# Performance work log

Measured on AMD Instinct MI355X. Metric: run time of the kernel, lower is better.

## Reference

```python
import jax, jax.numpy as jnp
import numpy as np

EPS = 1e-12  # matches torch F.normalize eps
TEMPERATURE = 1.0
LAMBDA = 0.8


def _l2norm(x):
    n = jnp.sqrt(jnp.sum(x * x, axis=-1, keepdims=True))
    return x / jnp.maximum(n, EPS)


def setup_inputs() -> dict:
    key = jax.random.key(0)
    feats = jax.random.normal(key, (4, 4096, 512), dtype=jnp.float32)
    return {"feats": feats, "node": 8}


def reference(feats, node):
    f = _l2norm(feats)                                   # [B,N,D]
    scores = jnp.einsum('bnd,bmd->bnm', f, f) / TEMPERATURE  # [B,N,N]
    vals, idx = jax.lax.top_k(scores, node)              # [B,N,k]
    B, N, _ = scores.shape
    bi = jnp.arange(B)[:, None, None]
    ni = jnp.arange(N)[None, :, None]
    sparse = jnp.full_like(scores, -jnp.inf).at[bi, ni, idx].set(vals)
    w = jax.nn.softmax(sparse, axis=-1)                  # zeros outside top-k
    feats_att = jnp.einsum('bnm,bmd->bnd', w, f)
    feats_gam = f * LAMBDA + feats_att * (1.0 - LAMBDA)
    return _l2norm(feats_gam)
```

## Files before the change

kernel.cpp:

```cpp
#include <hip/hip_runtime.h>
#include <stdint.h>

#define NROWS 4096
#define NDIM  512
#define TOPT  8
#define NLIST 16
#define NCAND 128
#define NRESC 12
#define KSEL  8

typedef __attribute__((ext_vector_type(8))) short short8;
typedef __attribute__((ext_vector_type(4))) float f32x4;

__device__ __forceinline__ unsigned short f2bf(float x) {
  unsigned int u = __float_as_uint(x);
  return (unsigned short)((u + 0x7fffu + ((u >> 16) & 1u)) >> 16);
}

__device__ __forceinline__ void gl_lds16(const void* g, void* l) {
  void* gnc = (void*)g;
  __builtin_amdgcn_global_load_lds(
      (__attribute__((address_space(1))) void*)gnc,
      (__attribute__((address_space(3))) void*)l, 16, 0, 0);
}

__device__ __forceinline__ void ins8(unsigned int (&tv)[TOPT], unsigned int k) {
#pragma unroll
  for (int j = 0; j < TOPT; ++j) {
    const unsigned int nt = tv[j] > k ? tv[j] : k;
    k = tv[j] > k ? k : tv[j];
    tv[j] = nt;
  }
}

__global__ __launch_bounds__(256) void k_norm(const float* __restrict__ in,
                                              float* __restrict__ fout,
                                              unsigned short* __restrict__ fbf) {
  const int row = blockIdx.x * 4 + (threadIdx.x >> 6);
  const int l = threadIdx.x & 63;
  const float4* src = reinterpret_cast<const float4*>(in + (size_t)row * NDIM);
  float4 a = src[l * 2], b = src[l * 2 + 1];
  float ss = a.x * a.x + a.y * a.y + a.z * a.z + a.w * a.w +
             b.x * b.x + b.y * b.y + b.z * b.z + b.w * b.w;
#pragma unroll
  for (int off = 32; off; off >>= 1) ss += __shfl_xor(ss, off, 64);
  const float inv = 1.0f / fmaxf(sqrtf(ss), 1e-12f);
  a.x *= inv; a.y *= inv; a.z *= inv; a.w *= inv;
  b.x *= inv; b.y *= inv; b.z *= inv; b.w *= inv;
  float4* dst = reinterpret_cast<float4*>(fout + (size_t)row * NDIM);
  dst[l * 2] = a; dst[l * 2 + 1] = b;
  uint4 ub;
  ub.x = (unsigned)f2bf(a.x) | ((unsigned)f2bf(a.y) << 16);
  ub.y = (unsigned)f2bf(a.z) | ((unsigned)f2bf(a.w) << 16);
  ub.z = (unsigned)f2bf(b.x) | ((unsigned)f2bf(b.y) << 16);
  ub.w = (unsigned)f2bf(b.z) | ((unsigned)f2bf(b.w) << 16);
  reinterpret_cast<uint4*>(fbf + (size_t)row * NDIM)[l] = ub;
}

__global__ __launch_bounds__(512, 4) void k_coarse(const unsigned short* __restrict__ fbf,
                                                   unsigned int* __restrict__ keys) {
  __shared__ alignas(16) union {
    struct { unsigned short A[128 * 64]; unsigned short B[128 * 64]; } st;
    unsigned short S[128 * 128];
  } sh;

  const int tid = threadIdx.x;
  const int w = tid >> 6, l = tid & 63;

  const int lin = blockIdx.x;
  const int xcd = lin & 7;
  const int slot = lin >> 3;
  const int xq = xcd * 4 + (slot & 3);
  const int ym = (slot >> 2) & 7;
  const int zb = slot >> 5;

  const int q0 = xq * 128;
  const int m0 = ym * 512;
  const int bbase = zb * NROWS;

  const int qh = w >> 2, mq = w & 3;
  const int r = tid >> 2, sub = tid & 3;
  const int rx = r & 31;

  const int lrow = (l >> 3);
  const int lkg  = ((l & 7) ^ lrow) * 8;

  unsigned int tv[TOPT];
#pragma unroll
  for (int j = 0; j < TOPT; ++j) tv[j] = 0u;

  const f32x4 vzero = {0.f, 0.f, 0.f, 0.f};

  for (int mt = 0; mt < 4; ++mt) {
    const int mbase = m0 + mt * 128;
    f32x4 acc[4][2];
#pragma unroll
    for (int i = 0; i < 4; ++i)
#pragma unroll
      for (int j = 0; j < 2; ++j) acc[i][j] = vzero;

    for (int kt = 0; kt < 8; ++kt) {
      const int kk = kt * 64;
#pragma unroll
      for (int t = 0; t < 2; ++t) {
        const int sa = w * 2 + t;
        const int srow = sa * 8 + lrow;
        gl_lds16(fbf + ((size_t)(bbase + q0 + srow) << 9) + kk + lkg,
                 &sh.st.A[sa * 512]);
        gl_lds16(fbf + ((size_t)(bbase + mbase + srow) << 9) + kk + lkg,
                 &sh.st.B[sa * 512]);
      }
      __syncthreads();
#pragma unroll
      for (int ks = 0; ks < 2; ++ks) {
        short8 av[4], bv[2];
        const int kgrp = ks * 4 + (l >> 4);
#pragma unroll
        for (int i = 0; i < 4; ++i) {
          const int row = qh * 64 + i * 16 + (l & 15);
          av[i] = *(const short8*)&sh.st.A[row * 64 + (kgrp ^ (l & 7)) * 8];
        }
#pragma unroll
        for (int j = 0; j < 2; ++j) {
          const int row = mq * 32 + j * 16 + (l & 15);
          bv[j] = *(const short8*)&sh.st.B[row * 64 + (kgrp ^ (l & 7)) * 8];
        }
#pragma unroll
        for (int i = 0; i < 4; ++i)
#pragma unroll
          for (int j = 0; j < 2; ++j)
            acc[i][j] = __builtin_amdgcn_mfma_f32_16x16x32_bf16(av[i], bv[j], acc[i][j], 0, 0, 0);
      }
      __syncthreads();
    }

#pragma unroll
    for (int i = 0; i < 4; ++i) {
      const int qb_ = qh * 64 + i * 16 + (l >> 4) * 4;
#pragma unroll
      for (int j = 0; j < 2; ++j) {
        const int mc = mq * 32 + j * 16 + (l & 15);
#pragma unroll
        for (int rr = 0; rr < 4; ++rr) {
          const int q = qb_ + rr;
          unsigned int uu = __float_as_uint(acc[i][j][rr]);
          uu ^= (unsigned int)(((int)uu) >> 31) | 0x80000000u;
          const int pg = ((mc >> 2) ^ (q & 31));
          sh.S[q * 128 + pg * 4 + (mc & 3)] = (unsigned short)(uu >> 16);
        }
      }
    }
    __syncthreads();

    {
      const int invb0 = 4095 - (mbase + sub * 32);
#pragma unroll 4
      for (int cg = 0; cg < 8; ++cg) {
        const int pg = (sub * 8 + cg) ^ rx;
        const ushort4 s4 = *(const ushort4*)&sh.S[r * 128 + pg * 4];
        const unsigned int invb = (unsigned int)(invb0 - cg * 4);
        const unsigned int k0 = ((unsigned int)s4.x << 16) | invb;
        const unsigned int k1 = ((unsigned int)s4.y << 16) | (invb - 1);
        const unsigned int k2 = ((unsigned int)s4.z << 16) | (invb - 2);
        const unsigned int k3 = ((unsigned int)s4.w << 16) | (invb - 3);
        if (k0 > tv[TOPT - 1]) ins8(tv, k0);
        if (k1 > tv[TOPT - 1]) ins8(tv, k1);
        if (k2 > tv[TOPT - 1]) ins8(tv, k2);
        if (k3 > tv[TOPT - 1]) ins8(tv, k3);
      }
    }
    __syncthreads();
  }

  unsigned int ov[TOPT];
#pragma unroll
  for (int j = 0; j < TOPT; ++j) ov[j] = __shfl_xor(tv[j], 1, 64);
  unsigned int mg[TOPT];
#pragma unroll
  for (int j = 0; j < TOPT; ++j) {
    const unsigned int o = ov[TOPT - 1 - j];
    mg[j] = tv[j] > o ? tv[j] : o;
  }

  if ((sub & 1) == 0) {
    const int list = ym * 2 + (sub >> 1);
    unsigned int* dst = keys + (((size_t)(bbase + q0 + r)) * NLIST + list) * TOPT;
    reinterpret_cast<uint4*>(dst)[0] = make_uint4(mg[0], mg[1], mg[2], mg[3]);
    reinterpret_cast<uint4*>(dst)[1] = make_uint4(mg[4], mg[5], mg[6], mg[7]);
  }
}

__global__ __launch_bounds__(256) void k_final(const float* __restrict__ f,
                                               const unsigned int* __restrict__ keys,
                                               float* __restrict__ out) {
  __shared__ int sh_si[4][NRESC];

  const int lin = blockIdx.x;
  const int xcd = lin & 7;
  const int slot = lin >> 3;
  const int b = xcd >> 1;
  const int wv = threadIdx.x >> 6;
  const int n = ((xcd & 1) * 512 + slot) * 4 + wv;
  const int qg = b * NROWS + n;
  const int l = threadIdx.x & 63;

  const uint2 kk = reinterpret_cast<const uint2*>(keys + (size_t)qg * NCAND)[l];
  const unsigned int ka = kk.x, kb = kk.y;

  unsigned int T = 0u;
#pragma unroll
  for (int bit = 31; bit >= 0; --bit) {
    const unsigned int Tp = T | (1u << bit);
    const int cnt = (int)__popcll(__ballot(ka >= Tp)) +
                    (int)__popcll(__ballot(kb >= Tp));
    T = (cnt >= NRESC) ? Tp : T;
  }

  {
    const unsigned long long mA = __ballot(ka >= T);
    const unsigned long long mB = __ballot(kb >= T);
    const unsigned long long lt = (1ull << l) - 1ull;
    if (ka >= T) sh_si[wv][(int)__popcll(mA & lt)] = 4095 - (int)(ka & 4095u);
    if (kb >= T) sh_si[wv][(int)__popcll(mA) + (int)__popcll(mB & lt)] =
        4095 - (int)(kb & 4095u);
  }
  asm volatile("s_waitcnt lgkmcnt(0)" ::: "memory");
  __builtin_amdgcn_sched_barrier(0);

  int si[NRESC];
#pragma unroll
  for (int j = 0; j < NRESC; ++j)
    si[j] = __builtin_amdgcn_readfirstlane(sh_si[wv][j]);

  const float* __restrict__ fb = f + (size_t)b * NROWS * NDIM;
  const float* frow = fb + (size_t)n * NDIM;
  float selfv[8];
#pragma unroll
  for (int c = 0; c < 8; ++c) selfv[c] = frow[c * 64 + l];

  double ex[NRESC];
#pragma unroll
  for (int rr = 0; rr < NRESC; ++rr) {
    const float* g = fb + (size_t)si[rr] * NDIM;
    double s = 0.0;
#pragma unroll
    for (int c = 0; c < 8; ++c) s += (double)selfv[c] * (double)g[c * 64 + l];
    ex[rr] = s;
  }
#pragma unroll
  for (int off = 32; off; off >>= 1) {
#pragma unroll
    for (int rr = 0; rr < NRESC; ++rr) ex[rr] += __shfl_xor(ex[rr], off, 64);
  }

  int rank_[NRESC];
#pragma unroll
  for (int j = 0; j < NRESC; ++j) {
    int rk = 0;
#pragma unroll
    for (int a = 0; a < NRESC; ++a) {
      if (a != j) {
        const bool beats = (ex[a] > ex[j]) || (ex[a] == ex[j] && si[a] < si[j]);
        rk += beats ? 1 : 0;
      }
    }
    rank_[j] = rk;
  }
  double mxd = ex[0];
#pragma unroll
  for (int j = 1; j < NRESC; ++j) mxd = ex[j] > mxd ? ex[j] : mxd;

  const float mxf = (float)mxd;
  float wj[NRESC];
  float wsum = 0.f;
#pragma unroll
  for (int j = 0; j < NRESC; ++j) {
    const float e = expf((float)ex[j] - mxf);
    wj[j] = (rank_[j] < KSEL) ? e : 0.f;
    wsum += wj[j];
  }
  const float cs = 0.2f / wsum;

  float acc[8];
#pragma unroll
  for (int c = 0; c < 8; ++c) acc[c] = 0.8f * selfv[c];
#pragma unroll
  for (int rr = 0; rr < NRESC; ++rr) {
    if (rank_[rr] < KSEL) {
      const float* g = fb + (size_t)si[rr] * NDIM;
      const float wr = cs * wj[rr];
#pragma unroll
      for (int c = 0; c < 8; ++c) acc[c] = fmaf(wr, g[c * 64 + l], acc[c]);
    }
  }

  float ss = 0.f;
#pragma unroll
  for (int c = 0; c < 8; ++c) ss += acc[c] * acc[c];
#pragma unroll
  for (int off = 32; off; off >>= 1) ss += __shfl_xor(ss, off, 64);
  const float inv = 1.0f / fmaxf(sqrtf(ss), 1e-12f);
  float* orow = out + (size_t)qg * NDIM;
#pragma unroll
  for (int c = 0; c < 8; ++c) orow[c * 64 + l] = acc[c] * inv;
}

extern "C" void kernel_launch(void* const* d_in, const int* in_sizes, int n_in,
                              void* d_out, int out_size, void* d_ws, size_t ws_size,
                              hipStream_t stream) {
  (void)in_sizes; (void)n_in; (void)out_size; (void)ws_size;
  const float* feats = (const float*)d_in[0];
  char* ws = (char*)d_ws;
  float*          fnorm = (float*)(ws);
  unsigned short* fbf   = (unsigned short*)(ws + 33554432);
  unsigned int*   keys  = (unsigned int*)(ws + 50331648);
  float* out = (float*)d_out;

  k_norm<<<dim3(4096), dim3(256), 0, stream>>>(feats, fnorm, fbf);
  k_coarse<<<dim3(1024), dim3(512), 0, stream>>>(fbf, keys);
  k_final<<<dim3(4096), dim3(256), 0, stream>>>(fnorm, keys, out);
}
```

Measured before the change: 306.0 us.

## Split final kernel into top-k selection and blend kernels

Splits the final kernel in two. The first kernel reranks candidates in double precision, picks the top 8 by repeated max selection instead of pairwise ranking, and writes index/weight pairs to workspace. The second kernel gathers the 8 neighbours and applies the blend and normalisation. This lowers register pressure and removes the rank-guarded branchy loop. The cost is an extra launch, a workspace round trip, and re-reading the self row.

```diff
diff --git a/kernel.cpp b/kernel.cpp
--- a/kernel.cpp
+++ b/kernel.cpp
@@ -190,9 +190,9 @@
   }
 }
 
-__global__ __launch_bounds__(256) void k_final(const float* __restrict__ f,
-                                               const unsigned int* __restrict__ keys,
-                                               float* __restrict__ out) {
+__global__ __launch_bounds__(256) void k_sel(const float* __restrict__ f,
+                                             const unsigned int* __restrict__ keys,
+                                             uint2* __restrict__ selw) {
   __shared__ int sh_si[4][NRESC];
 
   const int lin = blockIdx.x;
@@ -253,45 +253,61 @@
     for (int rr = 0; rr < NRESC; ++rr) ex[rr] += __shfl_xor(ex[rr], off, 64);
   }
 
-  int rank_[NRESC];
-#pragma unroll
-  for (int j = 0; j < NRESC; ++j) {
-    int rk = 0;
-#pragma unroll
-    for (int a = 0; a < NRESC; ++a) {
-      if (a != j) {
-        const bool beats = (ex[a] > ex[j]) || (ex[a] == ex[j] && si[a] < si[j]);
-        rk += beats ? 1 : 0;
+  unsigned mask = 0;
+  double wex[KSEL]; int wi[KSEL];
+#pragma unroll
+  for (int rr = 0; rr < KSEL; ++rr) {
+    double mv = -1.0e300; int midx = 0x7fffffff; int mslot = 0;
+#pragma unroll
+    for (int j = 0; j < NRESC; ++j) {
+      const bool avail = ((mask >> j) & 1u) == 0u;
+      if (avail && (ex[j] > mv || (ex[j] == mv && si[j] < midx))) {
+        mv = ex[j]; midx = si[j]; mslot = j;
       }
     }
-    rank_[j] = rk;
-  }
-  double mxd = ex[0];
-#pragma unroll
-  for (int j = 1; j < NRESC; ++j) mxd = ex[j] > mxd ? ex[j] : mxd;
-
-  const float mxf = (float)mxd;
-  float wj[NRESC];
+    mask |= 1u << mslot;
+    wex[rr] = mv; wi[rr] = midx;
+  }
+
+  float w8[KSEL];
+  const float mx = (float)wex[0];
   float wsum = 0.f;
 #pragma unroll
-  for (int j = 0; j < NRESC; ++j) {
-    const float e = expf((float)ex[j] - mxf);
-    wj[j] = (rank_[j] < KSEL) ? e : 0.f;
-    wsum += wj[j];
-  }
+  for (int rr = 0; rr < KSEL; ++rr) { w8[rr] = expf((float)wex[rr] - mx); wsum += w8[rr]; }
   const float cs = 0.2f / wsum;
 
+  uint2 osel = make_uint2(0u, 0u);
+#pragma unroll
+  for (int rr = 0; rr < KSEL; ++rr) {
+    if (l == rr) osel = make_uint2((unsigned)wi[rr], __float_as_uint(cs * w8[rr]));
+  }
+  if (l < KSEL) selw[(size_t)qg * KSEL + l] = osel;
+}
+
+__global__ __launch_bounds__(256) void k_blend(const float* __restrict__ f,
+                                               const uint2* __restrict__ selw,
+                                               float* __restrict__ out) {
+  const int row = blockIdx.x * 4 + (threadIdx.x >> 6);
+  const int b = row >> 12;
+  const int l = threadIdx.x & 63;
+
+  const uint2* pw = selw + (size_t)row * KSEL;
+  uint2 p[KSEL];
+#pragma unroll
+  for (int j = 0; j < KSEL; ++j) p[j] = pw[j];
+
+  const float* __restrict__ fb = f + (size_t)b * NROWS * NDIM;
+  const float* frow = f + (size_t)row * NDIM;
+
   float acc[8];
 #pragma unroll
-  for (int c = 0; c < 8; ++c) acc[c] = 0.8f * selfv[c];
-#pragma unroll
-  for (int rr = 0; rr < NRESC; ++rr) {
-    if (rank_[rr] < KSEL) {
-      const float* g = fb + (size_t)si[rr] * NDIM;
-      const float wr = cs * wj[rr];
-#pragma unroll
-      for (int c = 0; c < 8; ++c) acc[c] = fmaf(wr, g[c * 64 + l], acc[c]);
-    }
+  for (int c = 0; c < 8; ++c) acc[c] = 0.8f * frow[c * 64 + l];
+#pragma unroll
+  for (int j = 0; j < KSEL; ++j) {
+    const float* g = fb + (size_t)p[j].x * NDIM;
+    const float wr = __uint_as_float(p[j].y);
+#pragma unroll
+    for (int c = 0; c < 8; ++c) acc[c] = fmaf(wr, g[c * 64 + l], acc[c]);
   }
 
   float ss = 0.f;
@@ -300,7 +316,7 @@
 #pragma unroll
   for (int off = 32; off; off >>= 1) ss += __shfl_xor(ss, off, 64);
   const float inv = 1.0f / fmaxf(sqrtf(ss), 1e-12f);
-  float* orow = out + (size_t)qg * NDIM;
+  float* orow = out + (size_t)row * NDIM;
 #pragma unroll
   for (int c = 0; c < 8; ++c) orow[c * 64 + l] = acc[c] * inv;
 }
@@ -314,9 +330,11 @@
   float*          fnorm = (float*)(ws);
   unsigned short* fbf   = (unsigned short*)(ws + 33554432);
   unsigned int*   keys  = (unsigned int*)(ws + 50331648);
+  uint2*          selw  = (uint2*)(ws + 58720256);
   float* out = (float*)d_out;
 
-  k_norm<<<dim3(4096), dim3(256), 0, stream>>>(feats, fnorm, fbf);
+  k_norm <<<dim3(4096), dim3(256), 0, stream>>>(feats, fnorm, fbf);
   k_coarse<<<dim3(1024), dim3(512), 0, stream>>>(fbf, keys);
-  k_final<<<dim3(4096), dim3(256), 0, stream>>>(fnorm, keys, out);
-}
+  k_sel  <<<dim3(4096), dim3(256), 0, stream>>>(fnorm, keys, selw);
+  k_blend<<<dim3(4096), dim3(256), 0, stream>>>(fnorm, selw, out);
+}
```

Result: faster. 278.9 us (-8.9%).
